# Performance work log

Hardware: AMD Instinct MI355X
Metric: run time of the kernel (lower is better)

## Reference

```python
import jax, jax.numpy as jnp
import numpy as np
from jax import lax

NTAG = 31
HID = 100
NEG = -10000.0


def gru_dir(x, w_ih, w_hh, b_ih, b_hh):
    # x: [T, B, 100]; PyTorch gate order in weights: [r, z, n]
    B = x.shape[1]
    h0 = jnp.zeros((B, HID), dtype=x.dtype)

    def step(h, xt):
        gi = xt @ w_ih.T + b_ih          # [B, 3H]
        gh = h @ w_hh.T + b_hh           # [B, 3H]
        ir, iz, inn = jnp.split(gi, 3, axis=-1)
        hr, hz, hn = jnp.split(gh, 3, axis=-1)
        r = jax.nn.sigmoid(ir + hr)
        z = jax.nn.sigmoid(iz + hz)
        n = jnp.tanh(inn + r * hn)
        h = (1.0 - z) * n + z * h
        return h, h

    _, ys = lax.scan(step, h0, x)
    return ys                             # [T, B, H]


def viterbi(feats, msk, transitions):
    # feats: [T, 31], msk: [T], transitions[next, prev]
    init = jnp.full((NTAG,), NEG, dtype=feats.dtype).at[0].set(0.0)
    idx = jnp.arange(NTAG)

    def step(fv, inp):
        feat, m = inp
        scores = fv[None, :] + transitions       # [next, prev]
        bp = jnp.argmax(scores, axis=1)          # [31]
        vv = jnp.max(scores, axis=1) + feat      # [31]
        live = m > 0
        fv_new = jnp.where(live, vv, fv)
        bp = jnp.where(live, bp, idx)            # masked step: identity backpointer
        return fv_new, bp

    fv, bps = lax.scan(step, init, (feats, msk))
    final = jnp.argmax(fv)
    score = fv[final]

    def back(tag, bp):
        return bp[tag], tag

    _, path = lax.scan(back, final, bps, reverse=True)  # path[t] = tag at step t
    return score, path


def setup_inputs() -> dict:
    key = jax.random.key(0)
    ks = jax.random.split(key, 12)
    T, B, D = 2048, 128, 100
    s = 0.1  # ~ 1/sqrt(hidden)
    u = lambda k, sh: jax.random.uniform(k, sh, jnp.float32, -s, s)
    tr = jax.random.normal(ks[10], (NTAG, NTAG), jnp.float32)
    tr = tr.at[0, :].set(NEG).at[:, 29].set(NEG).at[:, 30].set(NEG)
    tr = tr.at[30, 30].set(0.0).at[29, 30].set(0.0)
    return {
        "sentence": jax.random.normal(ks[0], (T, B, D), jnp.float32),
        "mask": jnp.ones((B, T), jnp.float32),
        "w_ih_f": u(ks[1], (3 * HID, D)), "w_hh_f": u(ks[2], (3 * HID, HID)),
        "b_ih_f": u(ks[3], (3 * HID,)), "b_hh_f": u(ks[4], (3 * HID,)),
        "w_ih_b": u(ks[5], (3 * HID, D)), "w_hh_b": u(ks[6], (3 * HID, HID)),
        "b_ih_b": u(ks[7], (3 * HID,)), "b_hh_b": u(ks[8], (3 * HID,)),
        "w_out": u(ks[9], (NTAG, 2 * HID)), "b_out": jnp.zeros((NTAG,), jnp.float32),
        "transitions": tr,
        "batch": B,
        "seq": 0,
    }


def reference(sentence, mask, w_ih_f, w_hh_f, b_ih_f, b_hh_f,
              w_ih_b, w_hh_b, b_ih_b, b_hh_b, w_out, b_out,
              transitions, batch, seq):
    fwd = gru_dir(sentence, w_ih_f, w_hh_f, b_ih_f, b_hh_f)
    bwd = gru_dir(sentence[::-1], w_ih_b, w_hh_b, b_ih_b, b_hh_b)[::-1]
    gru_out = jnp.concatenate([fwd, bwd], axis=-1)        # [T, B, 200]
    feats = gru_out @ w_out.T + b_out                      # [T, B, 31]
    feats_b = jnp.transpose(feats, (1, 0, 2))              # [B, T, 31]
    score, path = viterbi(feats_b[seq], mask[seq], transitions)
    return score, path
```

## Files before the change

### kernel.cpp

```cpp
#include <hip/hip_runtime.h>
#include <stdint.h>

#define TT 2048
#define BB 128
#define DD 100
#define HH 100
#define GG 300
#define NT 31
#define NEGV (-10000.0f)

#define REP25(M) M(0) M(1) M(2) M(3) M(4) M(5) M(6) M(7) M(8) M(9) M(10) M(11) \
                 M(12) M(13) M(14) M(15) M(16) M(17) M(18) M(19) M(20) M(21) M(22) M(23) M(24)
#define REP31(M) M(0) M(1) M(2) M(3) M(4) M(5) M(6) M(7) M(8) M(9) M(10) M(11) \
                 M(12) M(13) M(14) M(15) M(16) M(17) M(18) M(19) M(20) M(21) M(22) M(23) \
                 M(24) M(25) M(26) M(27) M(28) M(29) M(30)
#define REP8(M)  M(0) M(1) M(2) M(3) M(4) M(5) M(6) M(7)

#define RL(v, k) __int_as_float(__builtin_amdgcn_readlane(__float_as_int(v), (k)))

typedef float f2 __attribute__((ext_vector_type(2)));

#define BARRIER_LGKM() do {                                   \
    __builtin_amdgcn_sched_barrier(0);                        \
    asm volatile("s_waitcnt lgkmcnt(0)" ::: "memory");        \
    __builtin_amdgcn_s_barrier();                             \
    __builtin_amdgcn_sched_barrier(0);                        \
} while (0)

__global__ __launch_bounds__(320) void gi_kernel(
    const float* __restrict__ sent, const int* __restrict__ seqp,
    const float* __restrict__ w_ih_f, const float* __restrict__ b_ih_f,
    const float* __restrict__ w_ih_b, const float* __restrict__ b_ih_b,
    float* __restrict__ gi)
{
    const int t   = blockIdx.x;
    const int dir = blockIdx.y;
    const int j   = threadIdx.x;
    const int seq = seqp[0];
    const int ts  = dir ? (TT - 1 - t) : t;
    __shared__ __align__(16) float x_s[DD];
    if (j < DD) x_s[j] = sent[((size_t)ts * BB + seq) * DD + j];
    __syncthreads();
    if (j < GG) {
        const float* w = dir ? w_ih_b : w_ih_f;
        const float* b = dir ? b_ih_b : b_ih_f;
        const float4* w4 = (const float4*)(w + j * DD);
        const float4* x4 = (const float4*)x_s;
        float a0 = 0.f, a1 = 0.f, a2 = 0.f, a3 = 0.f;
        #pragma unroll
        for (int k = 0; k < DD / 4; k++) {
            float4 wv = w4[k], xv = x4[k];
            a0 += wv.x * xv.x; a1 += wv.y * xv.y;
            a2 += wv.z * xv.z; a3 += wv.w * xv.w;
        }
        gi[((size_t)dir * TT + t) * GG + j] = b[j] + (a0 + a1) + (a2 + a3);
    }
}

__global__ __launch_bounds__(320, 1) void gru_seq_kernel(
    const float* __restrict__ gi,
    const float* __restrict__ w_hh_f, const float* __restrict__ b_hh_f,
    const float* __restrict__ w_hh_b, const float* __restrict__ b_hh_b,
    const float* __restrict__ w_out,
    float* __restrict__ pfeat)
{
    const int dir  = blockIdx.x;
    const int tid  = threadIdx.x;
    const int wave = tid >> 6, lane = tid & 63;
    const bool isdot = (wave < 4);
    const int q    = isdot ? wave : 0;
    const int k0   = q * 25;
    const float* w_hh = dir ? w_hh_b : w_hh_f;
    const float* b_hh = dir ? b_hh_b : b_hh_f;
    const float* gid  = gi + (size_t)dir * TT * GG;
    float* pf = pfeat + (size_t)dir * TT * NT;

    __shared__ __align__(16) float part[2][4][384];
    __shared__ __align__(16) float hsh[4 * 28];

    const int P0 = lane, P1 = 64 + lane, P2 = 128 + lane;
    const int hb = q * 28;

    auto rowp = [&](int s) -> const float* {
        if (s < GG) return w_hh + (size_t)s * DD + k0;
        int wr = s - GG; if (wr > NT - 1) wr = NT - 1;
        return w_out + (size_t)wr * (2 * HH) + dir * HH + k0;
    };
    const float* a0p = rowp(2 * P0);     const float* b0p = rowp(2 * P0 + 1);
    const float* a1p = rowp(2 * P1);     const float* b1p = rowp(2 * P1 + 1);
    const float* a2p = rowp(2 * P2);     const float* b2p = rowp(2 * P2 + 1);

    #define DECLW(i) f2 w0_##i = {0.f,0.f}, w1_##i = {0.f,0.f}, w2_##i = {0.f,0.f};
    REP25(DECLW)
    #define LDW(i) w0_##i.x = a0p[i]; w0_##i.y = b0p[i]; \
                   w1_##i.x = a1p[i]; w1_##i.y = b1p[i]; \
                   w2_##i.x = a2p[i]; w2_##i.y = b2p[i];
    if (isdot) { REP25(LDW) }

    const int r = k0 + lane;
    float bhr = 0.f, bhz = 0.f, bhn = 0.f;
    if (isdot && lane < 25) { bhr = b_hh[r]; bhz = b_hh[HH + r]; bhn = b_hh[2 * HH + r]; }

    const int  p     = lane;
    const bool is_pf = (!isdot) && (lane < NT);
    #define DECLPH(i) float ph##i = 0.f;
    REP8(DECLPH)

    float hreg = 0.f;
    if (isdot && lane < 25) hsh[hb + lane] = 0.f;

    float gAr = 0.f, gAz = 0.f, gAn = 0.f, gBr = 0.f, gBz = 0.f, gBn = 0.f;
    if (isdot && lane < 25) {
        gAr = gid[r];      gAz = gid[HH + r];      gAn = gid[2 * HH + r];
        gBr = gid[GG + r]; gBz = gid[GG + HH + r]; gBn = gid[GG + 2 * HH + r];
    }

    #define PKFMA_LO(ACC, W, H) asm("v_pk_fma_f32 %0, %1, %2, %0 op_sel:[0,0,0] op_sel_hi:[1,0,1]" \
                                    : "+v"(ACC) : "v"(W), "v"(H));
    #define PKFMA_HI(ACC, W, H) asm("v_pk_fma_f32 %0, %1, %2, %0 op_sel:[0,1,0] op_sel_hi:[1,1,1]" \
                                    : "+v"(ACC) : "v"(W), "v"(H));

    #define PAIRS(M) M(0,0,1) M(1,2,3) M(2,4,5) M(3,6,7) M(4,8,9) M(5,10,11) \
                     M(6,12,13) M(7,14,15) M(8,16,17) M(9,18,19) M(10,20,21) M(11,22,23)

    #define DOTP(s, ka, kb) { f2 hv = *(const f2*)&hsh[hb + 2 * (s)];        \
        PKFMA_LO(acc0, w0_##ka, hv) PKFMA_LO(acc1, w1_##ka, hv)              \
        PKFMA_LO(acc2, w2_##ka, hv)                                          \
        PKFMA_HI(acc0, w0_##kb, hv) PKFMA_HI(acc1, w1_##kb, hv)              \
        PKFMA_HI(acc2, w2_##kb, hv) }
    #define DOTLAST { f2 hv = *(const f2*)&hsh[hb + 24];                     \
        PKFMA_LO(acc0, w0_24, hv) PKFMA_LO(acc1, w1_24, hv)                  \
        PKFMA_LO(acc2, w2_24, hv) }

    #define GRU_STEP(TIDX, BUF, SLOT, cr, cz, cn) {                          \
        if (isdot) {                                                         \
            f2 acc0 = {0.f, 0.f}, acc1 = {0.f, 0.f}, acc2 = {0.f, 0.f};      \
            PAIRS(DOTP)                                                      \
            DOTLAST                                                          \
            *(f2*)&part[BUF][q][2 * P0] = acc0;                              \
            *(f2*)&part[BUF][q][2 * P1] = acc1;                              \
            *(f2*)&part[BUF][q][2 * P2] = acc2;                              \
        }                                                                    \
        BARRIER_LGKM();                                                      \
        if (isdot) {                                                         \
            __builtin_amdgcn_s_setprio(1);                                   \
            if (lane < 25) {                                                 \
                float pr = part[BUF][0][r] + part[BUF][1][r]                 \
                         + part[BUF][2][r] + part[BUF][3][r];                \
                float pz = part[BUF][0][HH + r] + part[BUF][1][HH + r]       \
                         + part[BUF][2][HH + r] + part[BUF][3][HH + r];      \
                float pn = part[BUF][0][2*HH + r] + part[BUF][1][2*HH + r]   \
                         + part[BUF][2][2*HH + r] + part[BUF][3][2*HH + r];  \
                float xr  = pr + bhr + (cr);                                 \
                float xz  = pz + bhz + (cz);                                 \
                float ghn = pn + bhn;                                        \
                float rr  = 1.f / (1.f + __expf(-xr));                       \
                float zz  = 1.f / (1.f + __expf(-xz));                       \
                float pre = (cn) + rr * ghn;                                 \
                pre = fmaxf(fminf(pre, 40.f), -40.f);                        \
                float e2  = __expf(-2.f * pre);                              \
                float nn  = (1.f - e2) / (1.f + e2);                         \
                hreg = (1.f - zz) * nn + zz * hreg;                          \
                hsh[hb + lane] = hreg;                                       \
                int tp = (TIDX) + 2; tp = (tp < TT) ? tp : (TT - 1);         \
                cr = gid[tp * GG + r];                                       \
                cz = gid[tp * GG + HH + r];                                  \
                cn = gid[tp * GG + 2 * HH + r];                              \
            }                                                                \
            __builtin_amdgcn_s_setprio(0);                                   \
        } else if (is_pf && (TIDX) > 0) {                                    \
            ph##SLOT = part[BUF][0][GG + p] + part[BUF][1][GG + p]           \
                     + part[BUF][2][GG + p] + part[BUF][3][GG + p];          \
        }                                                                    \
    }

    #define PHST(i) pf[(size_t)(dir ? (TT - 1 - (tb + i)) : (tb + i)) * NT + p] = ph##i;

    for (int tt = 0; tt < TT; tt += 8) {
        GRU_STEP(tt + 0, 0, 7, gAr, gAz, gAn)
        if (is_pf && tt >= 8) { int tb = tt - 8; REP8(PHST) }
        GRU_STEP(tt + 1, 1, 0, gBr, gBz, gBn)
        GRU_STEP(tt + 2, 0, 1, gAr, gAz, gAn)
        GRU_STEP(tt + 3, 1, 2, gBr, gBz, gBn)
        GRU_STEP(tt + 4, 0, 3, gAr, gAz, gAn)
        GRU_STEP(tt + 5, 1, 4, gBr, gBz, gBn)
        GRU_STEP(tt + 6, 0, 5, gAr, gAz, gAn)
        GRU_STEP(tt + 7, 1, 6, gBr, gBz, gBn)
    }

    {
        if (isdot) {
            f2 acc2e = {0.f, 0.f};
            #define DOT2P(s, ka, kb) { f2 hv = *(const f2*)&hsh[hb + 2 * (s)];   \
                PKFMA_LO(acc2e, w2_##ka, hv) PKFMA_HI(acc2e, w2_##kb, hv) }
            PAIRS(DOT2P)
            { f2 hv = *(const f2*)&hsh[hb + 24]; PKFMA_LO(acc2e, w2_24, hv) }
            *(f2*)&part[0][q][2 * P2] = acc2e;
        }
        BARRIER_LGKM();
        if (is_pf) {
            ph7 = part[0][0][GG + p] + part[0][1][GG + p]
                + part[0][2][GG + p] + part[0][3][GG + p];
            int tb = TT - 8;
            REP8(PHST)
        }
    }
}

__global__ __launch_bounds__(64) void vit_scan_kernel(
    const float* __restrict__ pfeat, const float* __restrict__ mask,
    const int* __restrict__ seqp, const float* __restrict__ trans,
    const float* __restrict__ b_out,
    float* __restrict__ fvg, int* __restrict__ meta, float* __restrict__ out)
{
    const int lane = threadIdx.x;
    const int ln   = (lane < NT) ? lane : (NT - 1);
    const float* mrow = mask + (size_t)seqp[0] * TT;
    const float* pff = pfeat;
    const float* pfb = pfeat + (size_t)TT * NT;

    #define DECLTR(i) float tr##i = trans[ln * NT + i];
    REP31(DECLTR)
    const float bo = b_out[ln];

    float fv = (lane == 0) ? 0.f : NEGV;
    fvg[lane] = fv;

    float ffr[8], fbr[8], mr[8];
    #pragma unroll
    for (int q = 0; q < 8; q++) {
        ffr[q] = pff[q * NT + ln]; fbr[q] = pfb[q * NT + ln]; mr[q] = mrow[q];
    }

    for (int t = 0; t < TT; t += 8) {
        #pragma unroll
        for (int q = 0; q < 8; q++) {
            float fcur = ffr[q] + fbr[q] + bo;
            float mcur = mr[q];
            int tp = t + q + 8; tp = (tp < TT) ? tp : (TT - 1);
            ffr[q] = pff[tp * NT + ln]; fbr[q] = pfb[tp * NT + ln]; mr[q] = mrow[tp];
            #define VADD(i) float v##i = RL(fv, i) + tr##i;
            REP31(VADD)
            #undef VADD
            float m0 = fmaxf(fmaxf(v0,  v1),  v2);
            float m1 = fmaxf(fmaxf(v3,  v4),  v5);
            float m2 = fmaxf(fmaxf(v6,  v7),  v8);
            float m3 = fmaxf(fmaxf(v9,  v10), v11);
            float m4 = fmaxf(fmaxf(v12, v13), v14);
            float m5 = fmaxf(fmaxf(v15, v16), v17);
            float m6 = fmaxf(fmaxf(v18, v19), v20);
            float m7 = fmaxf(fmaxf(v21, v22), v23);
            float m8 = fmaxf(fmaxf(v24, v25), v26);
            float m9 = fmaxf(fmaxf(v27, v28), v29);
            float n0 = fmaxf(fmaxf(m0, m1), m2);
            float n1 = fmaxf(fmaxf(m3, m4), m5);
            float n2 = fmaxf(fmaxf(m6, m7), m8);
            float m  = fmaxf(fmaxf(fmaxf(fmaxf(n0, n1), n2), m9), v30);
            float cand = m + fcur;
            fv = (mcur > 0.f) ? cand : fv;
            fvg[(t + q + 1) * 64 + lane] = fv;
        }
    }

    float fbest = RL(fv, 0);
    int ftag = 0;
    #pragma unroll
    for (int q = 1; q < NT; q++) {
        float s = RL(fv, q);
        if (s > fbest) { fbest = s; ftag = q; }
    }
    if (lane == 0) { out[0] = fbest; meta[0] = ftag; }
}

__global__ __launch_bounds__(1024) void vit_bp_kernel(
    const float* __restrict__ fvg, const float* __restrict__ mask,
    const int* __restrict__ seqp, const float* __restrict__ trans,
    uint8_t* __restrict__ bpg, uint8_t* __restrict__ gmapg)
{
    const int b    = blockIdx.x;
    const int tid  = threadIdx.x;
    const int wave = tid >> 6, lane = tid & 63;
    const int j    = lane & 31;
    const int jr   = (j < NT) ? j : (NT - 1);
    const float* mrow = mask + (size_t)seqp[0] * TT;

    __shared__ int bpl[64][32];

    float trj[NT];
    #pragma unroll
    for (int q = 0; q < NT; q++) trj[q] = trans[jr * NT + q];

    #pragma unroll
    for (int q4 = 0; q4 < 4; q4++) {
        const int t = b * 64 + wave * 4 + q4;
        float fvp = fvg[t * 64 + lane];
        float mcur = mrow[t];
        float best = RL(fvp, 0) + trj[0];
        int bi = 0;
        #pragma unroll
        for (int q = 1; q < NT; q++) {
            float s = RL(fvp, q) + trj[q];
            if (s > best) { best = s; bi = q; }
        }
        int bpn = (mcur > 0.f) ? bi : j;
        if (j == 31) bpn = 31;
        if (lane < 32) {
            bpl[wave * 4 + q4][lane] = bpn;
            if (j < NT) bpg[(size_t)t * NT + j] = (uint8_t)bpn;
        }
    }
    __syncthreads();
    if (wave == 0) {
        int G = j;
        for (int i = 0; i < 64; i++) {
            int bpv = bpl[i][j];
            G = __shfl(G, bpv);
        }
        if (lane < 32) gmapg[b * 32 + lane] = (uint8_t)G;
    }
}

__global__ __launch_bounds__(64) void vit_back_kernel(
    const uint8_t* __restrict__ bpg, const uint8_t* __restrict__ gmapg,
    const int* __restrict__ meta, float* __restrict__ out)
{
    const int tid = threadIdx.x;
    __shared__ uint8_t bps[TT * NT];
    __shared__ uint8_t gm[32 * 32];
    __shared__ uint8_t echk[32];

    const uint32_t* src = (const uint32_t*)bpg;
    uint32_t* dst = (uint32_t*)bps;
    for (int i = tid; i < TT * NT / 4; i += 64) dst[i] = src[i];
    for (int i = tid; i < 1024 / 4; i += 64)
        ((uint32_t*)gm)[i] = ((const uint32_t*)gmapg)[i];
    __syncthreads();

    if (tid == 0) {
        int tag = meta[0];
        for (int b = 31; b >= 0; b--) { echk[b] = (uint8_t)tag; tag = gm[b * 32 + tag]; }
    }
    __syncthreads();
    if (tid < 32) {
        int tag = echk[tid];
        for (int i = 63; i >= 0; i--) {
            int t = tid * 64 + i;
            out[1 + t] = (float)tag;
            tag = bps[t * NT + tag];
        }
    }
}

extern "C" void kernel_launch(void* const* d_in, const int* in_sizes, int n_in,
                              void* d_out, int out_size, void* d_ws, size_t ws_size,
                              hipStream_t stream) {
    const float* sent   = (const float*)d_in[0];
    const float* mask   = (const float*)d_in[1];
    const float* w_ih_f = (const float*)d_in[2];
    const float* w_hh_f = (const float*)d_in[3];
    const float* b_ih_f = (const float*)d_in[4];
    const float* b_hh_f = (const float*)d_in[5];
    const float* w_ih_b = (const float*)d_in[6];
    const float* w_hh_b = (const float*)d_in[7];
    const float* b_ih_b = (const float*)d_in[8];
    const float* b_hh_b = (const float*)d_in[9];
    const float* w_out  = (const float*)d_in[10];
    const float* b_out  = (const float*)d_in[11];
    const float* trans  = (const float*)d_in[12];
    const int*   seqp   = (const int*)d_in[14];
    float* out = (float*)d_out;

    float* gi    = (float*)d_ws;
    float* pfeat = gi + (size_t)2 * TT * GG;
    float* fvg   = pfeat + (size_t)2 * TT * NT;
    float* bpf   = fvg + (size_t)(TT + 1) * 64;
    uint8_t* bpg   = (uint8_t*)bpf;
    uint8_t* gmapg = bpg + (size_t)TT * NT;
    int*     meta  = (int*)(gmapg + 1024);

    gi_kernel<<<dim3(TT, 2), 320, 0, stream>>>(sent, seqp, w_ih_f, b_ih_f,
                                               w_ih_b, b_ih_b, gi);
    gru_seq_kernel<<<2, 320, 0, stream>>>(gi, w_hh_f, b_hh_f, w_hh_b, b_hh_b,
                                          w_out, pfeat);
    vit_scan_kernel<<<1, 64, 0, stream>>>(pfeat, mask, seqp, trans, b_out,
                                          fvg, meta, out);
    vit_bp_kernel<<<32, 1024, 0, stream>>>(fvg, mask, seqp, trans, bpg, gmapg);
    vit_back_kernel<<<1, 64, 0, stream>>>(bpg, gmapg, meta, out);
}
```

Measured before the change: 1.805 ms.

## Speculatively parallelize Viterbi forward scan with warmup chunks and verification fallback

Replaces the serial Viterbi max-plus scan with a speculative scheme. 32 blocks each run a 128-step warmup from a zero vector and then compute backpointers for their 64-step chunk in parallel. A serial chain kernel then rebuilds exact scores with only a shuffle per step, a parallel verify kernel checks every step against the full max, and a final kernel reruns the serial scan if any mismatch is found. This removes the 31-way max from the serial critical path, but adds extra kernel launches and risks a slow fallback when backpointers do not converge within the warmup.

```diff
diff --git a/kernel.cpp b/kernel.cpp
--- a/kernel.cpp
+++ b/kernel.cpp
@@ -11,9 +11,6 @@
 
 #define REP25(M) M(0) M(1) M(2) M(3) M(4) M(5) M(6) M(7) M(8) M(9) M(10) M(11) \
                  M(12) M(13) M(14) M(15) M(16) M(17) M(18) M(19) M(20) M(21) M(22) M(23) M(24)
-#define REP31(M) M(0) M(1) M(2) M(3) M(4) M(5) M(6) M(7) M(8) M(9) M(10) M(11) \
-                 M(12) M(13) M(14) M(15) M(16) M(17) M(18) M(19) M(20) M(21) M(22) M(23) \
-                 M(24) M(25) M(26) M(27) M(28) M(29) M(30)
 #define REP8(M)  M(0) M(1) M(2) M(3) M(4) M(5) M(6) M(7)
 
 #define RL(v, k) __int_as_float(__builtin_amdgcn_readlane(__float_as_int(v), (k)))
@@ -207,63 +204,190 @@
     }
 }
 
-__global__ __launch_bounds__(64) void vit_scan_kernel(
+__global__ __launch_bounds__(64) void vit_spec_kernel(
     const float* __restrict__ pfeat, const float* __restrict__ mask,
     const int* __restrict__ seqp, const float* __restrict__ trans,
-    const float* __restrict__ b_out,
-    float* __restrict__ fvg, int* __restrict__ meta, float* __restrict__ out)
-{
+    const float* __restrict__ b_out, uint8_t* __restrict__ bpg)
+{
+    const int b    = blockIdx.x;
     const int lane = threadIdx.x;
     const int ln   = (lane < NT) ? lane : (NT - 1);
     const float* mrow = mask + (size_t)seqp[0] * TT;
     const float* pff = pfeat;
     const float* pfb = pfeat + (size_t)TT * NT;
 
-    #define DECLTR(i) float tr##i = trans[ln * NT + i];
-    REP31(DECLTR)
+    float trk[NT];
+    #pragma unroll
+    for (int k = 0; k < NT; k++) trk[k] = trans[ln * NT + k];
     const float bo = b_out[ln];
 
+    int t0 = b * 64 - 128; if (t0 < 0) t0 = 0;
+    float fv;
+    if (t0 == 0) fv = (lane == 0) ? 0.f : NEGV;
+    else         fv = 0.f;
+    const int tstore = b * 64, tend = b * 64 + 64;
+
+    float ffc = pff[t0 * NT + ln], fbc = pfb[t0 * NT + ln], mc = mrow[t0];
+    for (int t = t0; t < tend; ++t) {
+        int tn = (t + 1 < tend) ? (t + 1) : t;
+        float ffn = pff[tn * NT + ln], fbn = pfb[tn * NT + ln], mn = mrow[tn];
+        float fcur = (ffc + fbc) + bo;
+        float best = RL(fv, 0) + trk[0];
+        int bi = 0;
+        #pragma unroll
+        for (int k = 1; k < NT; k++) {
+            float s = RL(fv, k) + trk[k];
+            if (s > best) { best = s; bi = k; }
+        }
+        float cand = best + fcur;
+        bool live = (mc > 0.f);
+        float nfv = live ? cand : fv;
+        int bpn = live ? bi : ln;
+        if (t >= tstore && lane < NT) bpg[(size_t)t * NT + lane] = (uint8_t)bpn;
+        fv = nfv; ffc = ffn; fbc = fbn; mc = mn;
+    }
+}
+
+__global__ __launch_bounds__(64) void vit_chain_kernel(
+    const float* __restrict__ pfeat, const float* __restrict__ mask,
+    const int* __restrict__ seqp, const float* __restrict__ trans,
+    const float* __restrict__ b_out, const uint8_t* __restrict__ bpg,
+    float* __restrict__ fvg, int* __restrict__ flag)
+{
+    const int lane = threadIdx.x;
+    const int j = (lane < NT) ? lane : (NT - 1);
+    const float* mrow = mask + (size_t)seqp[0] * TT;
+    const float* pff = pfeat;
+    const float* pfb = pfeat + (size_t)TT * NT;
+
+    __shared__ float trl[NT * NT];
+    for (int i = lane; i < NT * NT; i += 64) trl[i] = trans[i];
+    if (lane == 0) flag[0] = 0;
+    __syncthreads();
+
+    const float bo = b_out[j];
+    const int jb = j * NT;
     float fv = (lane == 0) ? 0.f : NEGV;
     fvg[lane] = fv;
 
-    float ffr[8], fbr[8], mr[8];
+    float ffr[8], fbr[8], mr[8]; int bpr[8];
     #pragma unroll
     for (int q = 0; q < 8; q++) {
-        ffr[q] = pff[q * NT + ln]; fbr[q] = pfb[q * NT + ln]; mr[q] = mrow[q];
+        ffr[q] = pff[q * NT + j]; fbr[q] = pfb[q * NT + j];
+        mr[q] = mrow[q];          bpr[q] = bpg[q * NT + j];
     }
 
     for (int t = 0; t < TT; t += 8) {
         #pragma unroll
         for (int q = 0; q < 8; q++) {
-            float fcur = ffr[q] + fbr[q] + bo;
-            float mcur = mr[q];
+            float fcur = (ffr[q] + fbr[q]) + bo;
+            float mc = mr[q];
+            int bpv = bpr[q];
             int tp = t + q + 8; tp = (tp < TT) ? tp : (TT - 1);
-            ffr[q] = pff[tp * NT + ln]; fbr[q] = pfb[tp * NT + ln]; mr[q] = mrow[tp];
-            #define VADD(i) float v##i = RL(fv, i) + tr##i;
-            REP31(VADD)
-            #undef VADD
-            float m0 = fmaxf(fmaxf(v0,  v1),  v2);
-            float m1 = fmaxf(fmaxf(v3,  v4),  v5);
-            float m2 = fmaxf(fmaxf(v6,  v7),  v8);
-            float m3 = fmaxf(fmaxf(v9,  v10), v11);
-            float m4 = fmaxf(fmaxf(v12, v13), v14);
-            float m5 = fmaxf(fmaxf(v15, v16), v17);
-            float m6 = fmaxf(fmaxf(v18, v19), v20);
-            float m7 = fmaxf(fmaxf(v21, v22), v23);
-            float m8 = fmaxf(fmaxf(v24, v25), v26);
-            float m9 = fmaxf(fmaxf(v27, v28), v29);
-            float n0 = fmaxf(fmaxf(m0, m1), m2);
-            float n1 = fmaxf(fmaxf(m3, m4), m5);
-            float n2 = fmaxf(fmaxf(m6, m7), m8);
-            float m  = fmaxf(fmaxf(fmaxf(fmaxf(n0, n1), n2), m9), v30);
-            float cand = m + fcur;
-            fv = (mcur > 0.f) ? cand : fv;
-            fvg[(t + q + 1) * 64 + lane] = fv;
-        }
-    }
-
-    float fbest = RL(fv, 0);
-    int ftag = 0;
+            ffr[q] = pff[tp * NT + j]; fbr[q] = pfb[tp * NT + j];
+            mr[q] = mrow[tp];          bpr[q] = bpg[tp * NT + j];
+            float fvb = __shfl(fv, bpv);
+            float trv = trl[jb + bpv];
+            float cand = (fvb + trv) + fcur;
+            fv = (mc > 0.f) ? cand : fv;
+            if (lane < 32) fvg[(size_t)(t + q + 1) * 64 + lane] = fv;
+        }
+    }
+}
+
+__global__ __launch_bounds__(1024) void vit_verify_kernel(
+    const float* __restrict__ fvg, const float* __restrict__ mask,
+    const int* __restrict__ seqp, const float* __restrict__ trans,
+    const float* __restrict__ pfeat, const float* __restrict__ b_out,
+    const uint8_t* __restrict__ bpg, int* __restrict__ flag)
+{
+    const int b = blockIdx.x, tid = threadIdx.x;
+    const int wave = tid >> 6, lane = tid & 63;
+    const int j = lane & 31;
+    const int jr = (j < NT) ? j : (NT - 1);
+    const float* mrow = mask + (size_t)seqp[0] * TT;
+    const float* pff = pfeat;
+    const float* pfb = pfeat + (size_t)TT * NT;
+
+    float trj[NT];
+    #pragma unroll
+    for (int q = 0; q < NT; q++) trj[q] = trans[jr * NT + q];
+    const float bo = b_out[jr];
+
+    int bad = 0;
+    #pragma unroll
+    for (int q4 = 0; q4 < 4; q4++) {
+        const int t = b * 64 + wave * 4 + q4;
+        float fvp = fvg[(size_t)t * 64 + lane];
+        float nxt = fvg[(size_t)(t + 1) * 64 + lane];
+        float mc = mrow[t];
+        float fcur = (pff[t * NT + jr] + pfb[t * NT + jr]) + bo;
+        float best = RL(fvp, 0) + trj[0];
+        int bi = 0;
+        #pragma unroll
+        for (int q = 1; q < NT; q++) {
+            float s = RL(fvp, q) + trj[q];
+            if (s > best) { best = s; bi = q; }
+        }
+        bool live = (mc > 0.f);
+        float expv = live ? (best + fcur) : fvp;
+        int   expb = live ? bi : j;
+        if (lane < NT) {
+            if (expv != nxt) bad = 1;
+            if (expb != (int)bpg[(size_t)t * NT + j]) bad = 1;
+            if (t == 0) { float e0 = (j == 0) ? 0.f : NEGV; if (fvp != e0) bad = 1; }
+        }
+    }
+    if (bad) atomicOr(flag, 1);
+}
+
+__global__ __launch_bounds__(64) void vit_final_kernel(
+    const float* __restrict__ pfeat, const float* __restrict__ mask,
+    const int* __restrict__ seqp, const float* __restrict__ trans,
+    const float* __restrict__ b_out, const int* __restrict__ flag,
+    float* __restrict__ fvg, uint8_t* __restrict__ bpg,
+    int* __restrict__ meta, float* __restrict__ out)
+{
+    const int lane = threadIdx.x;
+    const int ln = (lane < NT) ? lane : (NT - 1);
+    if (flag[0] == 0) {
+        float fv = fvg[(size_t)TT * 64 + lane];
+        float fbest = RL(fv, 0); int ftag = 0;
+        #pragma unroll
+        for (int q = 1; q < NT; q++) {
+            float s = RL(fv, q);
+            if (s > fbest) { fbest = s; ftag = q; }
+        }
+        if (lane == 0) { out[0] = fbest; meta[0] = ftag; }
+        return;
+    }
+    const float* mrow = mask + (size_t)seqp[0] * TT;
+    const float* pff = pfeat;
+    const float* pfb = pfeat + (size_t)TT * NT;
+    float trk[NT];
+    #pragma unroll
+    for (int k = 0; k < NT; k++) trk[k] = trans[ln * NT + k];
+    const float bo = b_out[ln];
+    float fv = (lane == 0) ? 0.f : NEGV;
+    fvg[lane] = fv;
+    for (int t = 0; t < TT; ++t) {
+        float fcur = (pff[t * NT + ln] + pfb[t * NT + ln]) + bo;
+        float mc = mrow[t];
+        float best = RL(fv, 0) + trk[0];
+        int bi = 0;
+        #pragma unroll
+        for (int k = 1; k < NT; k++) {
+            float s = RL(fv, k) + trk[k];
+            if (s > best) { best = s; bi = k; }
+        }
+        bool live = (mc > 0.f);
+        float cand = best + fcur;
+        fv = live ? cand : fv;
+        int bpn = live ? bi : ln;
+        if (lane < NT) bpg[(size_t)t * NT + lane] = (uint8_t)bpn;
+        fvg[(size_t)(t + 1) * 64 + lane] = fv;
+    }
+    float fbest = RL(fv, 0); int ftag = 0;
     #pragma unroll
     for (int q = 1; q < NT; q++) {
         float s = RL(fv, q);
@@ -272,51 +396,25 @@
     if (lane == 0) { out[0] = fbest; meta[0] = ftag; }
 }
 
-__global__ __launch_bounds__(1024) void vit_bp_kernel(
-    const float* __restrict__ fvg, const float* __restrict__ mask,
-    const int* __restrict__ seqp, const float* __restrict__ trans,
-    uint8_t* __restrict__ bpg, uint8_t* __restrict__ gmapg)
-{
-    const int b    = blockIdx.x;
-    const int tid  = threadIdx.x;
-    const int wave = tid >> 6, lane = tid & 63;
-    const int j    = lane & 31;
-    const int jr   = (j < NT) ? j : (NT - 1);
-    const float* mrow = mask + (size_t)seqp[0] * TT;
-
-    __shared__ int bpl[64][32];
-
-    float trj[NT];
-    #pragma unroll
-    for (int q = 0; q < NT; q++) trj[q] = trans[jr * NT + q];
-
-    #pragma unroll
-    for (int q4 = 0; q4 < 4; q4++) {
-        const int t = b * 64 + wave * 4 + q4;
-        float fvp = fvg[t * 64 + lane];
-        float mcur = mrow[t];
-        float best = RL(fvp, 0) + trj[0];
-        int bi = 0;
-        #pragma unroll
-        for (int q = 1; q < NT; q++) {
-            float s = RL(fvp, q) + trj[q];
-            if (s > best) { best = s; bi = q; }
-        }
-        int bpn = (mcur > 0.f) ? bi : j;
-        if (j == 31) bpn = 31;
-        if (lane < 32) {
-            bpl[wave * 4 + q4][lane] = bpn;
-            if (j < NT) bpg[(size_t)t * NT + j] = (uint8_t)bpn;
-        }
-    }
+__global__ __launch_bounds__(256) void vit_compose_kernel(
+    const uint8_t* __restrict__ bpg, uint8_t* __restrict__ gmapg)
+{
+    const int b = blockIdx.x, tid = threadIdx.x;
+    __shared__ uint8_t bpl[64][32];
+    for (int idx = tid; idx < 64 * NT; idx += 256) {
+        int i = idx / NT, jj = idx - i * NT;
+        bpl[i][jj] = bpg[(size_t)(b * 64 + i) * NT + jj];
+    }
+    if (tid < 64) bpl[tid][31] = 31;
     __syncthreads();
-    if (wave == 0) {
+    if (tid < 64) {
+        int j = tid & 31;
         int G = j;
         for (int i = 0; i < 64; i++) {
             int bpv = bpl[i][j];
             G = __shfl(G, bpv);
         }
-        if (lane < 32) gmapg[b * 32 + lane] = (uint8_t)G;
+        if (tid < 32) gmapg[b * 32 + tid] = (uint8_t)G;
     }
 }
 
@@ -377,13 +475,19 @@
     uint8_t* bpg   = (uint8_t*)bpf;
     uint8_t* gmapg = bpg + (size_t)TT * NT;
     int*     meta  = (int*)(gmapg + 1024);
+    int*     flag  = meta + 1;
 
     gi_kernel<<<dim3(TT, 2), 320, 0, stream>>>(sent, seqp, w_ih_f, b_ih_f,
                                                w_ih_b, b_ih_b, gi);
     gru_seq_kernel<<<2, 320, 0, stream>>>(gi, w_hh_f, b_hh_f, w_hh_b, b_hh_b,
                                           w_out, pfeat);
-    vit_scan_kernel<<<1, 64, 0, stream>>>(pfeat, mask, seqp, trans, b_out,
-                                          fvg, meta, out);
-    vit_bp_kernel<<<32, 1024, 0, stream>>>(fvg, mask, seqp, trans, bpg, gmapg);
+    vit_spec_kernel<<<32, 64, 0, stream>>>(pfeat, mask, seqp, trans, b_out, bpg);
+    vit_chain_kernel<<<1, 64, 0, stream>>>(pfeat, mask, seqp, trans, b_out,
+                                           bpg, fvg, flag);
+    vit_verify_kernel<<<32, 1024, 0, stream>>>(fvg, mask, seqp, trans, pfeat,
+                                               b_out, bpg, flag);
+    vit_final_kernel<<<1, 64, 0, stream>>>(pfeat, mask, seqp, trans, b_out,
+                                           flag, fvg, bpg, meta, out);
+    vit_compose_kernel<<<32, 256, 0, stream>>>(bpg, gmapg);
     vit_back_kernel<<<1, 64, 0, stream>>>(bpg, gmapg, meta, out);
 }
```

New measurement: 2.745 ms. 52.0% more time.
